# Kernel optimization log

Hardware: AMD Instinct MI355X
Metric: run time of the kernel (lower is better)

The kernel has to match this reference:

```python
import jax, jax.numpy as jnp
import numpy as np

DIM = 1024
H = 16
DH = DIM // H  # 64
B = 2
T = 2048
LEFT, RIGHT = 128, 128  # attention_window
CAUSAL = True
SCALE = 1.0 / float(np.sqrt(DH))


def rotate_half(x):
    x1, x2 = jnp.split(x, 2, axis=-1)
    return jnp.concatenate((-x2, x1), axis=-1)


def apply_rotary_pos_emb(pos, t):
    # pos: [b, t, dh] -> [b, 1, t, dh]; t: [b, h, t, dh]
    pos = pos[:, None]
    return t * jnp.cos(pos) + rotate_half(t) * jnp.sin(pos)


def setup_inputs() -> dict:
    key = jax.random.key(0)
    ks = jax.random.split(key, 6)
    s = 1.0 / np.sqrt(DIM)
    x = jax.random.normal(ks[0], (B, T, DIM), dtype=jnp.float32)
    attention_mask = jnp.ones((T, T), dtype=bool)
    rotary_emb = jax.random.normal(ks[1], (B, T, DH), dtype=jnp.float32)
    Wq = jax.random.normal(ks[2], (DIM, DIM), dtype=jnp.float32) * s
    Wk = jax.random.normal(ks[3], (DIM, DIM), dtype=jnp.float32) * s
    Wv = jax.random.normal(ks[4], (DIM, DIM), dtype=jnp.float32) * s
    Wo = jax.random.normal(ks[5], (DIM, DIM), dtype=jnp.float32) * s
    return {"x": x, "attention_mask": attention_mask, "rotary_emb": rotary_emb,
            "Wq": Wq, "Wk": Wk, "Wv": Wv, "Wo": Wo}


def _build_mask(attention_mask):
    # i = key/column index, j = query/row index (matches torch code)
    i = jnp.arange(T)[None, :]
    j = jnp.arange(T)[:, None]
    mask = (i >= j - LEFT) & (i <= j + RIGHT)  # sliding window
    if CAUSAL:
        mask = mask & (i <= j)  # tril
    return attention_mask & mask  # [T, T]


def reference(x, attention_mask, rotary_emb, Wq, Wk, Wv, Wo):
    b, t, d = x.shape
    # QKV projections (nn.Linear: x @ W.T), split heads: b t (h dh) -> b h t dh
    def proj(W):
        return (x @ W.T).reshape(b, t, H, DH).transpose(0, 2, 1, 3)
    q, k, v = proj(Wq), proj(Wk), proj(Wv)
    q = apply_rotary_pos_emb(rotary_emb, q)
    k = apply_rotary_pos_emb(rotary_emb, k)
    mask = _build_mask(attention_mask)  # [T, T]
    scores = jnp.einsum('bhqd,bhkd->bhqk', q, k) * SCALE
    neg = jnp.asarray(-1e9, scores.dtype)
    scores = jnp.where(mask, scores, neg)
    attn = jax.nn.softmax(scores, axis=-1)
    out = jnp.einsum('bhqk,bhkd->bhqd', attn, v)
    out = out.transpose(0, 2, 1, 3).reshape(b, t, d)  # b h t dh -> b t (h dh)
    return out @ Wo.T
```

## Files before the change

### kernel.cpp

```cpp
#include <hip/hip_runtime.h>
#include <hip/hip_bf16.h>
#include <cstdint>

#define DIMD 1024
#define NH 16
#define DHD 64
#define BB 2
#define TT 2048
#define MROWS (BB * TT)

typedef unsigned short u16;
typedef __attribute__((ext_vector_type(8))) __bf16 bf16x8;
typedef __attribute__((ext_vector_type(4))) float f32x4;

__device__ __forceinline__ float bf2f(u16 u) {
    union { unsigned int i; float f; } v; v.i = ((unsigned int)u) << 16; return v.f;
}
__device__ __forceinline__ u16 f2bf(float f) {
    union { float f; unsigned int i; } v; v.f = f;
    unsigned int u = v.i;
    unsigned int r = (u + 0x7fffu + ((u >> 16) & 1u)) >> 16;
    return (u16)r;
}
__device__ __forceinline__ int4 pack8(const float4& a, const float4& b) {
    union { int4 v; u16 u[8]; } t;
    t.u[0] = f2bf(a.x); t.u[1] = f2bf(a.y); t.u[2] = f2bf(a.z); t.u[3] = f2bf(a.w);
    t.u[4] = f2bf(b.x); t.u[5] = f2bf(b.y); t.u[6] = f2bf(b.z); t.u[7] = f2bf(b.w);
    return t.v;
}

__global__ __launch_bounds__(256) void gemm_qkv(const float* __restrict__ x,
                                                const float* __restrict__ Wq,
                                                const float* __restrict__ Wk,
                                                const float* __restrict__ Wv,
                                                u16* __restrict__ qb,
                                                u16* __restrict__ kb,
                                                u16* __restrict__ vb,
                                                const float* __restrict__ rot) {
    constexpr int Kd = 1024;
    constexpr int LDA = 40;
    __shared__ u16 As[64 * LDA];
    __shared__ u16 Bs[128 * LDA];

    const int tid = threadIdx.x;
    const int L   = tid & 63;
    const int w   = tid >> 6;
    const int m0  = blockIdx.y * 64;
    const int nG  = blockIdx.x * 128;
    const int wsel = nG >> 10;
    const int wcol = nG & 1023;

    const float* W = (wsel == 0) ? Wq : (wsel == 1) ? Wk : Wv;
    u16* C         = (wsel == 0) ? qb : (wsel == 1) ? kb : vb;

    const int srow = tid >> 2;
    const int skc  = (tid & 3) * 8;
    const float* Ag = x + (size_t)(m0 + srow) * Kd + skc;
    const float* Wg = W + (size_t)(wcol + srow) * Kd + skc;
    u16* Asw = &As[srow * LDA + skc];
    u16* Bsw = &Bs[srow * LDA + skc];

    const int r16  = L & 15;
    const int quad = L >> 4;
    const int q8   = quad * 8;

    f32x4 acc[4][2];
#pragma unroll
    for (int i = 0; i < 4; i++)
#pragma unroll
        for (int j = 0; j < 2; j++) acc[i][j] = f32x4{0.f, 0.f, 0.f, 0.f};

    float4 aa0 = *(const float4*)(Ag);
    float4 ab0 = *(const float4*)(Ag + 4);
    float4 wa0 = *(const float4*)(Wg);
    float4 wb0 = *(const float4*)(Wg + 4);
    float4 wa1 = *(const float4*)(Wg + 64 * Kd);
    float4 wb1 = *(const float4*)(Wg + 64 * Kd + 4);

    const int cb = (w >> 1) * 64 + (w & 1) * 16;

    for (int k0 = 0; k0 < Kd; k0 += 32) {
        __syncthreads();
        *(int4*)(Asw)            = pack8(aa0, ab0);
        *(int4*)(Bsw)            = pack8(wa0, wb0);
        *(int4*)(Bsw + 64 * LDA) = pack8(wa1, wb1);
        __syncthreads();

        if (k0 + 32 < Kd) {
            int kn = k0 + 32;
            aa0 = *(const float4*)(Ag + kn);
            ab0 = *(const float4*)(Ag + kn + 4);
            wa0 = *(const float4*)(Wg + kn);
            wb0 = *(const float4*)(Wg + kn + 4);
            wa1 = *(const float4*)(Wg + 64 * Kd + kn);
            wb1 = *(const float4*)(Wg + 64 * Kd + kn + 4);
        }

        bf16x8 af[4], bfr[2];
#pragma unroll
        for (int i = 0; i < 4; i++)
            af[i] = *(const bf16x8*)&As[(i * 16 + r16) * LDA + q8];
#pragma unroll
        for (int j = 0; j < 2; j++)
            bfr[j] = *(const bf16x8*)&Bs[(cb + j * 32 + r16) * LDA + q8];
#pragma unroll
        for (int mi = 0; mi < 4; mi++)
#pragma unroll
            for (int ni = 0; ni < 2; ni++)
                acc[mi][ni] = __builtin_amdgcn_mfma_f32_16x16x32_bf16(
                    af[mi], bfr[ni], acc[mi][ni], 0, 0, 0);
    }

    const int dbase = (w & 1) * 16 + r16;
    if (wsel < 2) {
#pragma unroll
        for (int mi = 0; mi < 4; mi++)
#pragma unroll
            for (int r = 0; r < 4; r++) {
                int row = m0 + mi * 16 + quad * 4 + r;
                float s0, c0, s1, c1;
                __sincosf(rot[row * DHD + dbase], &s0, &c0);
                __sincosf(rot[row * DHD + dbase + 32], &s1, &c1);
                float x0 = acc[mi][0][r], x1 = acc[mi][1][r];
                C[(size_t)row * DIMD + wcol + cb + r16]      = f2bf(x0 * c0 - x1 * s0);
                C[(size_t)row * DIMD + wcol + cb + 32 + r16] = f2bf(x1 * c1 + x0 * s1);
            }
    } else {
#pragma unroll
        for (int mi = 0; mi < 4; mi++)
#pragma unroll
            for (int r = 0; r < 4; r++) {
                int row = m0 + mi * 16 + quad * 4 + r;
                C[(size_t)row * DIMD + wcol + cb + r16]      = f2bf(acc[mi][0][r]);
                C[(size_t)row * DIMD + wcol + cb + 32 + r16] = f2bf(acc[mi][1][r]);
            }
    }
}

__global__ __launch_bounds__(256) void gemm_out(const u16* __restrict__ A,
                                                const float* __restrict__ W,
                                                float* __restrict__ C) {
    constexpr int Kd = 1024, Nd = 1024;
    constexpr int LDA = 40;
    __shared__ u16 As[64 * LDA];
    __shared__ u16 Bs[128 * LDA];

    const int tid = threadIdx.x;
    const int L   = tid & 63;
    const int w   = tid >> 6;
    const int m0  = blockIdx.y * 64;
    const int n0  = blockIdx.x * 128;

    const int srow = tid >> 2;
    const int skc  = (tid & 3) * 8;
    const u16*   Ag = A + (size_t)(m0 + srow) * Kd + skc;
    const float* Wg = W + (size_t)(n0 + srow) * Kd + skc;
    u16* Asw = &As[srow * LDA + skc];
    u16* Bsw = &Bs[srow * LDA + skc];

    const int r16  = L & 15;
    const int quad = L >> 4;
    const int q8   = quad * 8;

    f32x4 acc[4][2];
#pragma unroll
    for (int i = 0; i < 4; i++)
#pragma unroll
        for (int j = 0; j < 2; j++) acc[i][j] = f32x4{0.f, 0.f, 0.f, 0.f};

    int4   ah0 = *(const int4*)(Ag);
    float4 wa0 = *(const float4*)(Wg);
    float4 wb0 = *(const float4*)(Wg + 4);
    float4 wa1 = *(const float4*)(Wg + 64 * Kd);
    float4 wb1 = *(const float4*)(Wg + 64 * Kd + 4);

    const int cb = (w >> 1) * 64 + (w & 1) * 16;

    for (int k0 = 0; k0 < Kd; k0 += 32) {
        __syncthreads();
        *(int4*)(Asw)            = ah0;
        *(int4*)(Bsw)            = pack8(wa0, wb0);
        *(int4*)(Bsw + 64 * LDA) = pack8(wa1, wb1);
        __syncthreads();

        if (k0 + 32 < Kd) {
            int kn = k0 + 32;
            ah0 = *(const int4*)(Ag + kn);
            wa0 = *(const float4*)(Wg + kn);
            wb0 = *(const float4*)(Wg + kn + 4);
            wa1 = *(const float4*)(Wg + 64 * Kd + kn);
            wb1 = *(const float4*)(Wg + 64 * Kd + kn + 4);
        }

        bf16x8 af[4], bfr[2];
#pragma unroll
        for (int i = 0; i < 4; i++)
            af[i] = *(const bf16x8*)&As[(i * 16 + r16) * LDA + q8];
#pragma unroll
        for (int j = 0; j < 2; j++)
            bfr[j] = *(const bf16x8*)&Bs[(cb + j * 32 + r16) * LDA + q8];
#pragma unroll
        for (int mi = 0; mi < 4; mi++)
#pragma unroll
            for (int ni = 0; ni < 2; ni++)
                acc[mi][ni] = __builtin_amdgcn_mfma_f32_16x16x32_bf16(
                    af[mi], bfr[ni], acc[mi][ni], 0, 0, 0);
    }

#pragma unroll
    for (int mi = 0; mi < 4; mi++)
#pragma unroll
        for (int r = 0; r < 4; r++) {
            int row = m0 + mi * 16 + quad * 4 + r;
            C[(size_t)row * Nd + n0 + cb + r16]      = acc[mi][0][r];
            C[(size_t)row * Nd + n0 + cb + 32 + r16] = acc[mi][1][r];
        }
}

__global__ __launch_bounds__(256) void attn_kernel(const u16* __restrict__ Q,
                                                   const u16* __restrict__ K,
                                                   const u16* __restrict__ V,
                                                   u16* __restrict__ O) {
    constexpr int LDK = 72;
    constexpr int LDV = 200;
    __shared__ u16 Ks[192 * LDK];
    __shared__ u16 Qs[64 * LDK];
    __shared__ u16 VTs[64 * LDV];

    const int tid = threadIdx.x;
    const int L   = tid & 63;
    const int w   = tid >> 6;
    const int b   = blockIdx.z;
    const int h   = blockIdx.y;
    const int q0  = blockIdx.x * 64;
    const int kstart = q0 - 128;

    for (int i = tid; i < 512; i += 256) {
        int qr = i >> 3, c = (i & 7) * 8;
        int t = q0 + qr;
        *(int4*)&Qs[qr * LDK + c] =
            *(const int4*)&Q[(size_t)(b * TT + t) * DIMD + h * DHD + c];
    }
    for (int i = tid; i < 1536; i += 256) {
        int kr = i >> 3, c = (i & 7) * 8;
        int kk = kstart + kr;
        int4 val = make_int4(0, 0, 0, 0);
        if (kk >= 0)
            val = *(const int4*)&K[(size_t)(b * TT + kk) * DIMD + h * DHD + c];
        *(int4*)&Ks[kr * LDK + c] = val;
    }
    for (int i = tid; i < 1536; i += 256) {
        int kr = i >> 3, c = (i & 7) * 8;
        int kk = kstart + kr;
        union { int4 v; u16 u[8]; } tmp;
        tmp.v = make_int4(0, 0, 0, 0);
        if (kk >= 0)
            tmp.v = *(const int4*)&V[(size_t)(b * TT + kk) * DIMD + h * DHD + c];
#pragma unroll
        for (int j = 0; j < 8; j++) VTs[(c + j) * LDV + kr] = tmp.u[j];
    }
    __syncthreads();

    const int r16  = L & 15;
    const int quad = L >> 4;
    const int q8   = quad * 8;

    bf16x8 aq0 = *(const bf16x8*)&Qs[(w * 16 + r16) * LDK + q8];
    bf16x8 aq1 = *(const bf16x8*)&Qs[(w * 16 + r16) * LDK + 32 + q8];

    float st[12][4];
    float rmax[4] = {-1e30f, -1e30f, -1e30f, -1e30f};
    const float SC = 0.125f;

#pragma unroll
    for (int kt = 0; kt < 12; kt++) {
        bf16x8 bk0 = *(const bf16x8*)&Ks[(kt * 16 + r16) * LDK + q8];
        bf16x8 bk1 = *(const bf16x8*)&Ks[(kt * 16 + r16) * LDK + 32 + q8];
        f32x4 s = f32x4{0.f, 0.f, 0.f, 0.f};
        s = __builtin_amdgcn_mfma_f32_16x16x32_bf16(aq0, bk0, s, 0, 0, 0);
        s = __builtin_amdgcn_mfma_f32_16x16x32_bf16(aq1, bk1, s, 0, 0, 0);
        int ka = kstart + kt * 16 + r16;
#pragma unroll
        for (int r = 0; r < 4; r++) {
            int qa = q0 + w * 16 + quad * 4 + r;
            float sv = s[r] * SC;
            bool ok = (ka >= 0) && (ka <= qa) && (ka >= qa - 128);
            sv = ok ? sv : -1e30f;
            st[kt][r] = sv;
            rmax[r] = fmaxf(rmax[r], sv);
        }
    }
#pragma unroll
    for (int off = 8; off >= 1; off >>= 1)
#pragma unroll
        for (int r = 0; r < 4; r++)
            rmax[r] = fmaxf(rmax[r], __shfl_xor(rmax[r], off, 64));

    __syncthreads();

    u16* Ps = &Ks[w * 16 * LDV];
    float rsum[4] = {0.f, 0.f, 0.f, 0.f};
#pragma unroll
    for (int kt = 0; kt < 12; kt++)
#pragma unroll
        for (int r = 0; r < 4; r++) {
            float p = __expf(st[kt][r] - rmax[r]);
            rsum[r] += p;
            Ps[(quad * 4 + r) * LDV + kt * 16 + r16] = f2bf(p);
        }
#pragma unroll
    for (int off = 8; off >= 1; off >>= 1)
#pragma unroll
        for (int r = 0; r < 4; r++)
            rsum[r] += __shfl_xor(rsum[r], off, 64);
    float rinv[4];
#pragma unroll
    for (int r = 0; r < 4; r++) rinv[r] = 1.0f / rsum[r];

    __syncthreads();

    bf16x8 pa[6];
#pragma unroll
    for (int kc = 0; kc < 6; kc++)
        pa[kc] = *(const bf16x8*)&Ps[r16 * LDV + kc * 32 + q8];

#pragma unroll
    for (int nt = 0; nt < 4; nt++) {
        f32x4 acc = f32x4{0.f, 0.f, 0.f, 0.f};
#pragma unroll
        for (int kc = 0; kc < 6; kc++) {
            bf16x8 bv = *(const bf16x8*)&VTs[(nt * 16 + r16) * LDV + kc * 32 + q8];
            acc = __builtin_amdgcn_mfma_f32_16x16x32_bf16(pa[kc], bv, acc, 0, 0, 0);
        }
#pragma unroll
        for (int r = 0; r < 4; r++) {
            int qa = q0 + w * 16 + quad * 4 + r;
            O[(size_t)(b * TT + qa) * DIMD + h * DHD + nt * 16 + r16] =
                f2bf(acc[r] * rinv[r]);
        }
    }
}

extern "C" void kernel_launch(void* const* d_in, const int* in_sizes, int n_in,
                              void* d_out, int out_size, void* d_ws, size_t ws_size,
                              hipStream_t stream) {
    const float* x   = (const float*)d_in[0];
    const float* rot = (const float*)d_in[2];
    const float* Wq  = (const float*)d_in[3];
    const float* Wk  = (const float*)d_in[4];
    const float* Wv  = (const float*)d_in[5];
    const float* Wo  = (const float*)d_in[6];
    float* out = (float*)d_out;

    u16* qb = (u16*)d_ws;
    u16* kb = qb + (size_t)MROWS * DIMD;
    u16* vb = kb + (size_t)MROWS * DIMD;
    u16* ab = vb + (size_t)MROWS * DIMD;

    gemm_qkv<<<dim3(3 * DIMD / 128, MROWS / 64), 256, 0, stream>>>(
        x, Wq, Wk, Wv, qb, kb, vb, rot);
    attn_kernel<<<dim3(TT / 64, NH, BB), 256, 0, stream>>>(qb, kb, vb, ab);
    gemm_out<<<dim3(DIMD / 128, MROWS / 64), 256, 0, stream>>>(ab, Wo, out);
}
```

Measured before the change: 209.9 us.

## Pre-convert inputs to bf16 and stage GEMM tiles via direct global-to-LDS loads

Adds a conversion kernel that turns x and all four weight matrices into bf16 buffers once per call. Both GEMMs then load bf16 tiles straight into shared memory with global_load_lds, which drops per-tile float conversion and register staging. The QKV GEMM also grows to 128x128 tiles with a 4x4 MFMA grid per wave. The cost is an extra launch plus a round trip through memory for the converted data, and the new LDS layout has no padding and no register prefetch overlap, so bank conflicts and load stalls may appear.

```diff
diff --git a/kernel.cpp b/kernel.cpp
--- a/kernel.cpp
+++ b/kernel.cpp
@@ -10,6 +10,7 @@
 #define MROWS (BB * TT)
 
 typedef unsigned short u16;
+typedef unsigned int u32;
 typedef __attribute__((ext_vector_type(8))) __bf16 bf16x8;
 typedef __attribute__((ext_vector_type(4))) float f32x4;
 
@@ -28,81 +29,169 @@
     t.u[4] = f2bf(b.x); t.u[5] = f2bf(b.y); t.u[6] = f2bf(b.z); t.u[7] = f2bf(b.w);
     return t.v;
 }
-
-__global__ __launch_bounds__(256) void gemm_qkv(const float* __restrict__ x,
-                                                const float* __restrict__ Wq,
-                                                const float* __restrict__ Wk,
-                                                const float* __restrict__ Wv,
+__device__ __forceinline__ void gl_lds16(const u16* g, u16* l) {
+    __builtin_amdgcn_global_load_lds(
+        (const __attribute__((address_space(1))) u32*)g,
+        (__attribute__((address_space(3))) u32*)l, 16, 0, 0);
+}
+
+__global__ __launch_bounds__(256) void convert_all(const float* __restrict__ x,
+                                                   const float* __restrict__ Wq,
+                                                   const float* __restrict__ Wk,
+                                                   const float* __restrict__ Wv,
+                                                   const float* __restrict__ Wo,
+                                                   u16* __restrict__ xb,
+                                                   u16* __restrict__ wqkv,
+                                                   u16* __restrict__ wob) {
+    int t = blockIdx.x * 256 + threadIdx.x;
+    const float* src; u16* dst; int rel;
+    if (t < 524288)      { src = x;  dst = xb;             rel = t; }
+    else if (t < 655360) { src = Wq; dst = wqkv;           rel = t - 524288; }
+    else if (t < 786432) { src = Wk; dst = wqkv + 1048576; rel = t - 655360; }
+    else if (t < 917504) { src = Wv; dst = wqkv + 2097152; rel = t - 786432; }
+    else                 { src = Wo; dst = wob;            rel = t - 917504; }
+    size_t e = (size_t)rel * 8;
+    float4 a = *(const float4*)(src + e);
+    float4 b = *(const float4*)(src + e + 4);
+    *(int4*)(dst + e) = pack8(a, b);
+}
+
+__global__ __launch_bounds__(256) void gemm_qkv(const u16* __restrict__ xb,
+                                                const u16* __restrict__ wqkv,
                                                 u16* __restrict__ qb,
                                                 u16* __restrict__ kb,
                                                 u16* __restrict__ vb,
                                                 const float* __restrict__ rot) {
     constexpr int Kd = 1024;
-    constexpr int LDA = 40;
-    __shared__ u16 As[64 * LDA];
-    __shared__ u16 Bs[128 * LDA];
-
-    const int tid = threadIdx.x;
-    const int L   = tid & 63;
-    const int w   = tid >> 6;
-    const int m0  = blockIdx.y * 64;
-    const int nG  = blockIdx.x * 128;
-    const int wsel = nG >> 10;
-    const int wcol = nG & 1023;
-
-    const float* W = (wsel == 0) ? Wq : (wsel == 1) ? Wk : Wv;
-    u16* C         = (wsel == 0) ? qb : (wsel == 1) ? kb : vb;
-
-    const int srow = tid >> 2;
-    const int skc  = (tid & 3) * 8;
-    const float* Ag = x + (size_t)(m0 + srow) * Kd + skc;
-    const float* Wg = W + (size_t)(wcol + srow) * Kd + skc;
-    u16* Asw = &As[srow * LDA + skc];
-    u16* Bsw = &Bs[srow * LDA + skc];
-
-    const int r16  = L & 15;
-    const int quad = L >> 4;
+    __shared__ u16 As[128 * 32];
+    __shared__ u16 Bs[128 * 32];
+
+    const int tid  = threadIdx.x;
+    const int lane = tid & 63;
+    const int w    = tid >> 6;
+    const int m0   = blockIdx.y * 128;
+    const int n0   = blockIdx.x * 128;
+
+    const u16* Ag = xb   + (size_t)(m0 + 32 * w + (lane >> 2)) * Kd + (lane & 3) * 8;
+    const u16* Bg = wqkv + (size_t)(n0 + 32 * w + (lane & 63) / 4) * Kd + (lane & 3) * 8;
+    u16* Al0 = &As[(32 * w) * 32];
+    u16* Al1 = &As[(32 * w + 16) * 32];
+    u16* Bl0 = &Bs[(32 * w) * 32];
+    u16* Bl1 = &Bs[(32 * w + 16) * 32];
+
+    const int r16  = lane & 15;
+    const int quad = lane >> 4;
     const int q8   = quad * 8;
-
-    f32x4 acc[4][2];
+    const int wm   = (w >> 1) * 64;
+    const int wn   = (w & 1) * 64;
+
+    f32x4 acc[4][4];
 #pragma unroll
     for (int i = 0; i < 4; i++)
 #pragma unroll
-        for (int j = 0; j < 2; j++) acc[i][j] = f32x4{0.f, 0.f, 0.f, 0.f};
-
-    float4 aa0 = *(const float4*)(Ag);
-    float4 ab0 = *(const float4*)(Ag + 4);
-    float4 wa0 = *(const float4*)(Wg);
-    float4 wb0 = *(const float4*)(Wg + 4);
-    float4 wa1 = *(const float4*)(Wg + 64 * Kd);
-    float4 wb1 = *(const float4*)(Wg + 64 * Kd + 4);
-
-    const int cb = (w >> 1) * 64 + (w & 1) * 16;
+        for (int j = 0; j < 4; j++) acc[i][j] = f32x4{0.f, 0.f, 0.f, 0.f};
 
     for (int k0 = 0; k0 < Kd; k0 += 32) {
         __syncthreads();
-        *(int4*)(Asw)            = pack8(aa0, ab0);
-        *(int4*)(Bsw)            = pack8(wa0, wb0);
-        *(int4*)(Bsw + 64 * LDA) = pack8(wa1, wb1);
+        gl_lds16(Ag + k0, Al0);
+        gl_lds16(Ag + 16 * Kd + k0, Al1);
+        gl_lds16(Bg + k0, Bl0);
+        gl_lds16(Bg + 16 * Kd + k0, Bl1);
         __syncthreads();
 
-        if (k0 + 32 < Kd) {
-            int kn = k0 + 32;
-            aa0 = *(const float4*)(Ag + kn);
-            ab0 = *(const float4*)(Ag + kn + 4);
-            wa0 = *(const float4*)(Wg + kn);
-            wb0 = *(const float4*)(Wg + kn + 4);
-            wa1 = *(const float4*)(Wg + 64 * Kd + kn);
-            wb1 = *(const float4*)(Wg + 64 * Kd + kn + 4);
-        }
+        bf16x8 af[4], bfr[4];
+#pragma unroll
+        for (int i = 0; i < 4; i++)
+            af[i] = *(const bf16x8*)&As[(wm + i * 16 + r16) * 32 + q8];
+#pragma unroll
+        for (int j = 0; j < 4; j++)
+            bfr[j] = *(const bf16x8*)&Bs[(wn + j * 16 + r16) * 32 + q8];
+#pragma unroll
+        for (int mi = 0; mi < 4; mi++)
+#pragma unroll
+            for (int ni = 0; ni < 4; ni++)
+                acc[mi][ni] = __builtin_amdgcn_mfma_f32_16x16x32_bf16(
+                    af[mi], bfr[ni], acc[mi][ni], 0, 0, 0);
+    }
+
+    const int wsel = n0 >> 10;
+    const int nloc = (n0 & 1023) + wn;
+    u16* C = (wsel == 0) ? qb : (wsel == 1) ? kb : vb;
+
+    if (wsel < 2) {
+#pragma unroll
+        for (int mi = 0; mi < 4; mi++)
+#pragma unroll
+            for (int r = 0; r < 4; r++) {
+                int row = m0 + wm + mi * 16 + quad * 4 + r;
+#pragma unroll
+                for (int ni = 0; ni < 2; ni++) {
+                    int d = ni * 16 + r16;
+                    float s0, c0, s1, c1;
+                    __sincosf(rot[row * DHD + d], &s0, &c0);
+                    __sincosf(rot[row * DHD + d + 32], &s1, &c1);
+                    float x0 = acc[mi][ni][r], x1 = acc[mi][ni + 2][r];
+                    C[(size_t)row * DIMD + nloc + d]      = f2bf(x0 * c0 - x1 * s0);
+                    C[(size_t)row * DIMD + nloc + d + 32] = f2bf(x1 * c1 + x0 * s1);
+                }
+            }
+    } else {
+#pragma unroll
+        for (int mi = 0; mi < 4; mi++)
+#pragma unroll
+            for (int ni = 0; ni < 4; ni++)
+#pragma unroll
+                for (int r = 0; r < 4; r++) {
+                    int row = m0 + wm + mi * 16 + quad * 4 + r;
+                    C[(size_t)row * DIMD + nloc + ni * 16 + r16] = f2bf(acc[mi][ni][r]);
+                }
+    }
+}
+
+__global__ __launch_bounds__(256) void gemm_out(const u16* __restrict__ A,
+                                                const u16* __restrict__ Wb,
+                                                float* __restrict__ C) {
+    constexpr int Kd = 1024, Nd = 1024;
+    __shared__ u16 As[64 * 32];
+    __shared__ u16 Bs[128 * 32];
+
+    const int tid  = threadIdx.x;
+    const int lane = tid & 63;
+    const int w    = tid >> 6;
+    const int m0   = blockIdx.y * 64;
+    const int n0   = blockIdx.x * 128;
+
+    const u16* Ag = A  + (size_t)(m0 + 16 * w + (lane >> 2)) * Kd + (lane & 3) * 8;
+    const u16* Bg = Wb + (size_t)(n0 + 32 * w + (lane >> 2)) * Kd + (lane & 3) * 8;
+    u16* Al  = &As[(16 * w) * 32];
+    u16* Bl0 = &Bs[(32 * w) * 32];
+    u16* Bl1 = &Bs[(32 * w + 16) * 32];
+
+    const int r16  = lane & 15;
+    const int quad = lane >> 4;
+    const int q8   = quad * 8;
+    const int cb   = (w >> 1) * 64 + (w & 1) * 16;
+
+    f32x4 acc[4][2];
+#pragma unroll
+    for (int i = 0; i < 4; i++)
+#pragma unroll
+        for (int j = 0; j < 2; j++) acc[i][j] = f32x4{0.f, 0.f, 0.f, 0.f};
+
+    for (int k0 = 0; k0 < Kd; k0 += 32) {
+        __syncthreads();
+        gl_lds16(Ag + k0, Al);
+        gl_lds16(Bg + k0, Bl0);
+        gl_lds16(Bg + 16 * Kd + k0, Bl1);
+        __syncthreads();
 
         bf16x8 af[4], bfr[2];
 #pragma unroll
         for (int i = 0; i < 4; i++)
-            af[i] = *(const bf16x8*)&As[(i * 16 + r16) * LDA + q8];
+            af[i] = *(const bf16x8*)&As[(i * 16 + r16) * 32 + q8];
 #pragma unroll
         for (int j = 0; j < 2; j++)
-            bfr[j] = *(const bf16x8*)&Bs[(cb + j * 32 + r16) * LDA + q8];
+            bfr[j] = *(const bf16x8*)&Bs[(cb + j * 32 + r16) * 32 + q8];
 #pragma unroll
         for (int mi = 0; mi < 4; mi++)
 #pragma unroll
@@ -111,110 +200,15 @@
                     af[mi], bfr[ni], acc[mi][ni], 0, 0, 0);
     }
 
-    const int dbase = (w & 1) * 16 + r16;
-    if (wsel < 2) {
-#pragma unroll
-        for (int mi = 0; mi < 4; mi++)
+#pragma unroll
+    for (int mi = 0; mi < 4; mi++)
+#pragma unroll
+        for (int j = 0; j < 2; j++)
 #pragma unroll
             for (int r = 0; r < 4; r++) {
                 int row = m0 + mi * 16 + quad * 4 + r;
-                float s0, c0, s1, c1;
-                __sincosf(rot[row * DHD + dbase], &s0, &c0);
-                __sincosf(rot[row * DHD + dbase + 32], &s1, &c1);
-                float x0 = acc[mi][0][r], x1 = acc[mi][1][r];
-                C[(size_t)row * DIMD + wcol + cb + r16]      = f2bf(x0 * c0 - x1 * s0);
-                C[(size_t)row * DIMD + wcol + cb + 32 + r16] = f2bf(x1 * c1 + x0 * s1);
+                C[(size_t)row * Nd + n0 + cb + j * 32 + r16] = acc[mi][j][r];
             }
-    } else {
-#pragma unroll
-        for (int mi = 0; mi < 4; mi++)
-#pragma unroll
-            for (int r = 0; r < 4; r++) {
-                int row = m0 + mi * 16 + quad * 4 + r;
-                C[(size_t)row * DIMD + wcol + cb + r16]      = f2bf(acc[mi][0][r]);
-                C[(size_t)row * DIMD + wcol + cb + 32 + r16] = f2bf(acc[mi][1][r]);
-            }
-    }
-}
-
-__global__ __launch_bounds__(256) void gemm_out(const u16* __restrict__ A,
-                                                const float* __restrict__ W,
-                                                float* __restrict__ C) {
-    constexpr int Kd = 1024, Nd = 1024;
-    constexpr int LDA = 40;
-    __shared__ u16 As[64 * LDA];
-    __shared__ u16 Bs[128 * LDA];
-
-    const int tid = threadIdx.x;
-    const int L   = tid & 63;
-    const int w   = tid >> 6;
-    const int m0  = blockIdx.y * 64;
-    const int n0  = blockIdx.x * 128;
-
-    const int srow = tid >> 2;
-    const int skc  = (tid & 3) * 8;
-    const u16*   Ag = A + (size_t)(m0 + srow) * Kd + skc;
-    const float* Wg = W + (size_t)(n0 + srow) * Kd + skc;
-    u16* Asw = &As[srow * LDA + skc];
-    u16* Bsw = &Bs[srow * LDA + skc];
-
-    const int r16  = L & 15;
-    const int quad = L >> 4;
-    const int q8   = quad * 8;
-
-    f32x4 acc[4][2];
-#pragma unroll
-    for (int i = 0; i < 4; i++)
-#pragma unroll
-        for (int j = 0; j < 2; j++) acc[i][j] = f32x4{0.f, 0.f, 0.f, 0.f};
-
-    int4   ah0 = *(const int4*)(Ag);
-    float4 wa0 = *(const float4*)(Wg);
-    float4 wb0 = *(const float4*)(Wg + 4);
-    float4 wa1 = *(const float4*)(Wg + 64 * Kd);
-    float4 wb1 = *(const float4*)(Wg + 64 * Kd + 4);
-
-    const int cb = (w >> 1) * 64 + (w & 1) * 16;
-
-    for (int k0 = 0; k0 < Kd; k0 += 32) {
-        __syncthreads();
-        *(int4*)(Asw)            = ah0;
-        *(int4*)(Bsw)            = pack8(wa0, wb0);
-        *(int4*)(Bsw + 64 * LDA) = pack8(wa1, wb1);
-        __syncthreads();
-
-        if (k0 + 32 < Kd) {
-            int kn = k0 + 32;
-            ah0 = *(const int4*)(Ag + kn);
-            wa0 = *(const float4*)(Wg + kn);
-            wb0 = *(const float4*)(Wg + kn + 4);
-            wa1 = *(const float4*)(Wg + 64 * Kd + kn);
-            wb1 = *(const float4*)(Wg + 64 * Kd + kn + 4);
-        }
-
-        bf16x8 af[4], bfr[2];
-#pragma unroll
-        for (int i = 0; i < 4; i++)
-            af[i] = *(const bf16x8*)&As[(i * 16 + r16) * LDA + q8];
-#pragma unroll
-        for (int j = 0; j < 2; j++)
-            bfr[j] = *(const bf16x8*)&Bs[(cb + j * 32 + r16) * LDA + q8];
-#pragma unroll
-        for (int mi = 0; mi < 4; mi++)
-#pragma unroll
-            for (int ni = 0; ni < 2; ni++)
-                acc[mi][ni] = __builtin_amdgcn_mfma_f32_16x16x32_bf16(
-                    af[mi], bfr[ni], acc[mi][ni], 0, 0, 0);
-    }
-
-#pragma unroll
-    for (int mi = 0; mi < 4; mi++)
-#pragma unroll
-        for (int r = 0; r < 4; r++) {
-            int row = m0 + mi * 16 + quad * 4 + r;
-            C[(size_t)row * Nd + n0 + cb + r16]      = acc[mi][0][r];
-            C[(size_t)row * Nd + n0 + cb + 32 + r16] = acc[mi][1][r];
-        }
 }
 
 __global__ __launch_bounds__(256) void attn_kernel(const u16* __restrict__ Q,
@@ -352,13 +346,17 @@
     const float* Wo  = (const float*)d_in[6];
     float* out = (float*)d_out;
 
-    u16* qb = (u16*)d_ws;
-    u16* kb = qb + (size_t)MROWS * DIMD;
-    u16* vb = kb + (size_t)MROWS * DIMD;
-    u16* ab = vb + (size_t)MROWS * DIMD;
-
-    gemm_qkv<<<dim3(3 * DIMD / 128, MROWS / 64), 256, 0, stream>>>(
-        x, Wq, Wk, Wv, qb, kb, vb, rot);
+    u16* xb   = (u16*)d_ws;
+    u16* wqkv = xb + 4194304;
+    u16* wob  = wqkv + 3145728;
+    u16* qb   = wob + 1048576;
+    u16* kb   = qb + 4194304;
+    u16* vb   = kb + 4194304;
+    u16* ab   = vb + 4194304;
+
+    convert_all<<<4096, 256, 0, stream>>>(x, Wq, Wk, Wv, Wo, xb, wqkv, wob);
+    gemm_qkv<<<dim3(3 * DIMD / 128, MROWS / 128), 256, 0, stream>>>(
+        xb, wqkv, qb, kb, vb, rot);
     attn_kernel<<<dim3(TT / 64, NH, BB), 256, 0, stream>>>(qb, kb, vb, ab);
-    gemm_out<<<dim3(DIMD / 128, MROWS / 64), 256, 0, stream>>>(ab, Wo, out);
-}
+    gemm_out<<<dim3(DIMD / 128, MROWS / 64), 256, 0, stream>>>(ab, wob, out);
+}
```

Result: faster. 185.4 us (-11.7%).
